# Kernel optimization log

Hardware: AMD Instinct MI355X
Metric: run time of the kernel (lower is better)

Reference implementation:

```python
import jax, jax.numpy as jnp
import numpy as np

TILE = 16
CLIP_NEAR, CLIP_FAR = 0.01, 10.0


def _sqrt_keepnan(x):
    # forward: sqrt(x) for x>0, NaN otherwise (matches torch.sqrt on negatives);
    # double-where keeps gradients finite.
    pos = x > 0
    return jnp.where(pos, jnp.sqrt(jnp.where(pos, x, 1.0)), jnp.nan)


def _quat_to_rot(q):
    # faithful to the source _quat_to_rot (including its sign quirks)
    x, y, z, w = q[:, 0], q[:, 1], q[:, 2], q[:, 3]
    r0 = jnp.stack([1 - 2 * (y * y + z * z), 2 * (x * y - w * z), 2 * (x * z + w * y)], -1)
    r1 = jnp.stack([2 * (x * y + w * z), 1 - 2 * (x * x - z * z), 2 * (y * z - w * x)], -1)
    r2 = jnp.stack([2 * (x * z + w * y), 2 * (y * z + w * x), 1 - 2 * (x * x + y * y)], -1)
    return jnp.stack([r0, r1, r2], -2)  # (N,3,3)


def _forward(mu, scales, quats, cols, opcs, viewmat, focal, H, W):
    N = mu.shape[0]
    fx = fy = float(focal)
    cx, cy = W / 2.0, H / 2.0
    n_, f_ = CLIP_NEAR, CLIP_FAR

    # --- project gaussians ---
    t = viewmat @ jnp.concatenate([mu.T, jnp.ones((1, N), mu.dtype)], 0)  # (4,N) camera space
    tp0 = (2.0 * fx / W) * t[0]
    tp1 = (2.0 * fy / H) * t[1]
    tp2 = ((f_ + n_) / (f_ - n_)) * t[2] + (-2.0 * f_ * n_ / (f_ - n_)) * t[3]
    tp3 = t[2]
    xys = jnp.stack([W * tp0 / tp3 / 2 + cx, H * tp1 / tp3 / 2 + cy], 1)  # (N,2)
    depths = tp2

    R = _quat_to_rot(quats)
    RS = R * scales[:, None, :]              # R @ diag(s)
    Sigma = RS @ jnp.swapaxes(RS, 1, 2)      # (N,3,3)
    tz = t[2]
    zz = jnp.zeros_like(tz)
    J = jnp.stack([
        jnp.stack([fx / tz, zz, -fx * t[0] / tz ** 2], -1),
        jnp.stack([zz, fy / tz, -fy * t[1] / tz ** 2], -1)], -2)  # (N,2,3)
    Rcw = viewmat[:3, :3]
    M = jnp.einsum('nij,jk->nik', J, Rcw)
    covs = jnp.einsum('nij,njk,nlk->nil', M, Sigma, M)  # (N,2,2)

    ind = jnp.argsort(depths)                # depth sort (front-to-back)
    xys, covs = xys[ind], covs[ind]
    cols_s, opcs_s = cols[ind], opcs[ind]

    # --- bounding boxes -> tile membership mask ---
    a, b, d = covs[:, 0, 0], covs[:, 0, 1], covs[:, 1, 1]
    Aev = jnp.sqrt(a * a - 2 * a * d + 4 * b * b + d * d)
    Bev = a + d
    l1, l2 = 0.5 * (Aev + Bev), 0.5 * (Bev - Aev)
    r1 = 3.0 * _sqrt_keepnan(l1)
    r2 = 3.0 * _sqrt_keepnan(l2)
    mx, my = xys[:, 0], xys[:, 1]
    corners = jnp.stack([
        jnp.stack([mx - r1, my + r2], -1),
        jnp.stack([mx + r1, my + r2], -1),
        jnp.stack([mx + r1, my - r2], -1),
        jnp.stack([mx - r1, my - r2], -1)], 1)  # (N,4,2)
    theta = jnp.where(b != 0, jnp.arctan2(l1 - a, b),
                      jnp.where(a >= d, jnp.pi / 2, 0.0))
    cth, sth = jnp.cos(theta), jnp.sin(theta)
    rot = jnp.stack([jnp.stack([cth, -sth], -1), jnp.stack([sth, cth], -1)], -2)
    bm = corners.mean(1, keepdims=True)
    bbs = jnp.einsum('nij,nkj->nki', rot, corners - bm) + bm
    bbs = jnp.where(jnp.isnan(bbs), -1.0, bbs)
    Wt, Ht = W // TILE, H // TILE
    xmin = jnp.clip(jnp.floor(bbs[:, :, 0].min(1) / TILE), 0, Wt - 1).astype(jnp.int32)
    xmax = jnp.clip(jnp.ceil(bbs[:, :, 0].max(1) / TILE), 0, Wt - 1).astype(jnp.int32)
    ymin = jnp.clip(jnp.floor(bbs[:, :, 1].min(1) / TILE), 0, Ht - 1).astype(jnp.int32)
    ymax = jnp.clip(jnp.ceil(bbs[:, :, 1].max(1) / TILE), 0, Ht - 1).astype(jnp.int32)
    txi = jnp.arange(Wt)
    tyi = jnp.arange(Ht)
    tmask = ((txi[None, None, :] >= xmin[:, None, None]) & (txi[None, None, :] <= xmax[:, None, None]) &
             (tyi[None, :, None] >= ymin[:, None, None]) & (tyi[None, :, None] <= ymax[:, None, None]))  # (N,Ht,Wt)
    pmask = jnp.moveaxis(jnp.repeat(jnp.repeat(tmask, TILE, 1), TILE, 2), 0, -1)  # (H,W,N)

    # --- rasterize: per-pixel gaussian eval + sorted alpha compositing ---
    e = 1e-6
    det = (a + e) * (d + e) - covs[:, 0, 1] * covs[:, 1, 0]
    i00 = (d + e) / det
    i01 = -covs[:, 0, 1] / det
    i10 = -covs[:, 1, 0] / det
    i11 = (a + e) / det
    px = jnp.arange(W, dtype=mu.dtype)
    py = jnp.arange(H, dtype=mu.dtype)
    dx = px[None, :, None] - mx[None, None, :]   # (1,W,N)
    dy = py[:, None, None] - my[None, None, :]   # (H,1,N)
    quad = dx * (i00 * dx + i01 * dy) + dy * (i10 * dx + i11 * dy)  # (H,W,N)
    Pg = jnp.nan_to_num(jnp.exp(-0.5 * quad))
    O = jax.nn.sigmoid(jax.nn.sigmoid(opcs_s))   # double sigmoid: faithful to source
    alpha = O[None, None, :] * Pg
    alpha = jnp.where(pmask, alpha, 0.0)         # only gaussians binned to this tile
    alpha = jnp.where(alpha < 0.001, 0.0, alpha)
    alpha = jnp.minimum(alpha, 0.99)
    trans = jnp.cumprod(1.0 - alpha, -1)         # inclusive transmittance
    Dtr = jnp.concatenate([jnp.ones((H, W, 1), alpha.dtype), trans[..., :-1]], -1)
    C = jnp.clip(cols_s, 1e-4, 1.0)
    rgb = jnp.clip(jnp.einsum('hwn,nc->hwc', alpha * Dtr, C), 1e-4, 1.0)
    nonempty = jnp.repeat(jnp.repeat(tmask.any(0), TILE, 0), TILE, 1)  # empty tiles stay 0
    return jnp.where(nonempty[..., None], rgb, 0.0)


def setup_inputs() -> dict:
    key = jax.random.key(0)
    ks = jax.random.split(key, 6)
    N, H, W = 512, 256, 256
    mu = jax.random.normal(ks[0], (N, 3), jnp.float32)
    scales = jax.random.uniform(ks[1], (N, 3), jnp.float32) * 0.05 + 0.01
    q = jax.random.normal(ks[2], (N, 4), jnp.float32)
    quats = q / jnp.linalg.norm(q, axis=1, keepdims=True)
    cols = jax.random.uniform(ks[3], (N, 3), jnp.float32)
    opcs = jax.random.normal(ks[4], (N,), jnp.float32)
    viewmat = jnp.array([[1, 0, 0, 0], [0, 1, 0, 0], [0, 0, 1, 5.0], [0, 0, 0, 1]], jnp.float32)
    gt = jax.random.uniform(ks[5], (H, W, 3), jnp.float32)
    return {"mu": mu, "scales": scales, "quats": quats, "cols": cols, "opcs": opcs,
            "viewmat": viewmat, "gt": gt, "focal": 200, "H": H, "W": W}


def reference(mu, scales, quats, cols, opcs, viewmat, gt, focal, H, W):
    # gt is accepted (matches source signature) but unused by forward
    return _forward(mu, scales, quats, cols, opcs, viewmat, focal, H, W)
```

## Files before the change

kernel.cpp:

```cpp
#include <hip/hip_runtime.h>
#include <math.h>
#include <float.h>

#define NMAX 512
#define TILE 16
#define FDIV(a,b) __fdividef((a),(b))

__global__ __launch_bounds__(1024) void fused_kernel(
    const float* __restrict__ mu, const float* __restrict__ scales,
    const float* __restrict__ quats, const float* __restrict__ cols,
    const float* __restrict__ opcs, const float* __restrict__ vm,
    const int* __restrict__ focal_p, const int* __restrict__ H_p,
    const int* __restrict__ W_p, float* __restrict__ out, int N)
{
    __shared__ float s_mx[NMAX], s_my[NMAX];
    __shared__ float s_q00[NMAX], s_qs[NMAX], s_q11[NMAX];
    __shared__ float s_O[NMAX], s_c0[NMAX], s_c1[NMAX], s_c2[NMAX];
    __shared__ float4 s_rs0[NMAX], s_rs1[NMAX], s_rs2[NMAX];
    __shared__ unsigned long long s_lk[NMAX];
    __shared__ int s_ord[NMAX];
    __shared__ float4 s_part[3][256];
    __shared__ int s_bc[16];

    const int lt = threadIdx.x;
    const int lane = lt & 63, w = lt >> 6;
    const int tx = blockIdx.x, ty = blockIdx.y;

    const int   Wi = W_p[0], Hi = H_p[0];
    const float fx = (float)focal_p[0];
    const float fy = fx;
    const float Wf = (float)Wi, Hf = (float)Hi;
    const float cxf = (float)((double)Wi / 2.0);
    const float cyf = (float)((double)Hi / 2.0);
    const float sxc = (float)(2.0 * (double)fx / (double)Wi);
    const float syc = (float)(2.0 * (double)fy / (double)Hi);
    const float dc1 = (float)((10.0 + 0.01) / (10.0 - 0.01));
    const float dc2 = (float)(-2.0 * 10.0 * 0.01 / (10.0 - 0.01));
    const int Wt = Wi / TILE, Ht = Hi / TILE;

    bool covered = false;
    unsigned int key = 0;
    float t0, t1, t2, M00, M01, M02, M10, M11, M12, mx, my;

    if (lt >= 512) {
        const int g2 = lt - 512;
        if (g2 < N) {
            const float4 q = ((const float4*)quats)[g2];
            const float qx = q.x, qy = q.y, qz = q.z, qw = q.w;
            const float R00 = 1.0f - 2.0f*(qy*qy + qz*qz);
            const float R01 = 2.0f*(qx*qy - qw*qz);
            const float R02 = 2.0f*(qx*qz + qw*qy);
            const float R10 = 2.0f*(qx*qy + qw*qz);
            const float R11 = 1.0f - 2.0f*(qx*qx - qz*qz);
            const float R12 = 2.0f*(qy*qz - qw*qx);
            const float R20 = 2.0f*(qx*qz + qw*qy);
            const float R21 = 2.0f*(qy*qz + qw*qx);
            const float R22 = 1.0f - 2.0f*(qx*qx + qy*qy);

            const float s0 = scales[3*g2], s1 = scales[3*g2+1], s2 = scales[3*g2+2];
            s_rs0[g2] = make_float4(R00*s0, R01*s1, R02*s2, 0.0f);
            s_rs1[g2] = make_float4(R10*s0, R11*s1, R12*s2, 0.0f);
            s_rs2[g2] = make_float4(R20*s0, R21*s1, R22*s2, 0.0f);

            const float op  = opcs[g2];
            const float sg1 = FDIV(1.0f, 1.0f + __expf(-op));
            s_O [g2] = FDIV(1.0f, 1.0f + __expf(-sg1));
            s_c0[g2] = fminf(fmaxf(cols[3*g2    ], 1e-04f), 1.0f);
            s_c1[g2] = fminf(fmaxf(cols[3*g2 + 1], 1e-04f), 1.0f);
            s_c2[g2] = fminf(fmaxf(cols[3*g2 + 2], 1e-04f), 1.0f);
        }
    } else {
        const int g = lt;
        if (g < N) {
            const float m0 = mu[3*g], m1 = mu[3*g+1], m2 = mu[3*g+2];
            t0 = vm[0]*m0  + vm[1]*m1  + vm[2]*m2  + vm[3];
            t1 = vm[4]*m0  + vm[5]*m1  + vm[6]*m2  + vm[7];
            t2 = vm[8]*m0  + vm[9]*m1  + vm[10]*m2 + vm[11];
            const float t3 = vm[12]*m0 + vm[13]*m1 + vm[14]*m2 + vm[15];

            const float depth = dc1 * t2 + dc2 * t3;
            unsigned int ub = __float_as_uint(depth);
            key = (ub & 0x80000000u) ? ~ub : (ub | 0x80000000u);

            const float itz = FDIV(1.0f, t2);
            mx = (Wf * (sxc * t0)) * itz * 0.5f + cxf;
            my = (Hf * (syc * t1)) * itz * 0.5f + cyf;

            const float J00 = fx * itz;
            const float J02 = -fx * t0 * itz * itz;
            const float J11 = fy * itz;
            const float J12 = -fy * t1 * itz * itz;
            M00 = J00*vm[0] + J02*vm[8];
            M01 = J00*vm[1] + J02*vm[9];
            M02 = J00*vm[2] + J02*vm[10];
            M10 = J11*vm[4] + J12*vm[8];
            M11 = J11*vm[5] + J12*vm[9];
            M12 = J11*vm[6] + J12*vm[10];
        }
    }
    __syncthreads();

    if (lt < 512 && lt < N) {
        const int g = lt;
        const float4 A0 = s_rs0[g], A1 = s_rs1[g], A2 = s_rs2[g];
        const float B00 = M00*A0.x + M01*A1.x + M02*A2.x;
        const float B01 = M00*A0.y + M01*A1.y + M02*A2.y;
        const float B02 = M00*A0.z + M01*A1.z + M02*A2.z;
        const float B10 = M10*A0.x + M11*A1.x + M12*A2.x;
        const float B11 = M10*A0.y + M11*A1.y + M12*A2.y;
        const float B12 = M10*A0.z + M11*A1.z + M12*A2.z;
        const float a = B00*B00 + B01*B01 + B02*B02;
        const float b = B00*B10 + B01*B11 + B02*B12;
        const float d = B10*B10 + B11*B11 + B12*B12;

        const float Aev = sqrtf(a*a - 2.0f*a*d + 4.0f*b*b + d*d);
        const float Bev = a + d;
        const float l1 = 0.5f * (Aev + Bev);
        const float l2 = 0.5f * (Bev - Aev);
        const float r1 = (l1 > 0.0f) ? 3.0f * sqrtf(l1) : NAN;
        const float r2 = (l2 > 0.0f) ? 3.0f * sqrtf(l2) : NAN;

        float cth, sth;
        if (b != 0.0f) {
            const float yv = l1 - a;
            const float ih = __frsqrt_rn(b*b + yv*yv);
            cth = b  * ih;
            sth = yv * ih;
        } else if (a >= d) {
            cth = -4.371139e-8f;
            sth = 1.0f;
        } else {
            cth = 1.0f;
            sth = 0.0f;
        }

        const float u  = mx - r1, v  = mx + r1;
        const float r_ = my + r2, s_ = my - r2;
        const float bmx = (((u + v) + v) + u) * 0.25f;
        const float bmy = (((r_ + r_) + s_) + s_) * 0.25f;
        const float pxo = u - bmx, qxo = v - bmx;
        const float ryo = r_ - bmy, syo = s_ - bmy;

        const float Axp = cth * pxo, Axq = cth * qxo;
        const float Bxr = (-sth) * ryo, Bxs = (-sth) * syo;
        float xmn  = (fminf(Axp, Axq) + fminf(Bxr, Bxs)) + bmx;
        float xmxv = (fmaxf(Axp, Axq) + fmaxf(Bxr, Bxs)) + bmx;
        const float Ayp = sth * pxo, Ayq = sth * qxo;
        const float Byr = cth * ryo, Bys = cth * syo;
        float ymn  = (fminf(Ayp, Ayq) + fminf(Byr, Bys)) + bmy;
        float ymxv = (fmaxf(Ayp, Ayq) + fmaxf(Byr, Bys)) + bmy;
        if (isnan(xmxv)) { xmn = -1.0f; xmxv = -1.0f; }
        if (isnan(ymxv)) { ymn = -1.0f; ymxv = -1.0f; }

        const int xmin = (int)fminf(fmaxf(floorf(xmn  * 0.0625f), 0.0f), (float)(Wt - 1));
        const int xmax = (int)fminf(fmaxf(ceilf (xmxv * 0.0625f), 0.0f), (float)(Wt - 1));
        const int ymin = (int)fminf(fmaxf(floorf(ymn  * 0.0625f), 0.0f), (float)(Ht - 1));
        const int ymax = (int)fminf(fmaxf(ceilf (ymxv * 0.0625f), 0.0f), (float)(Ht - 1));

        const float e = 1e-06f;
        const float det = (a + e) * (d + e) - b * b;
        const float idet = FDIV(1.0f, det);

        s_mx [g] = mx;
        s_my [g] = my;
        s_q00[g] = -0.5f * (d + e) * idet;
        s_qs [g] = b * idet;
        s_q11[g] = -0.5f * (a + e) * idet;

        covered = (tx >= xmin) & (tx <= xmax) & (ty >= ymin) & (ty <= ymax);
    }

    const unsigned long long word = __ballot(covered);
    if (lane == 0) s_bc[w] = __popcll(word);
    __syncthreads();

    int base = 0, M = 0;
    #pragma unroll
    for (int i = 0; i < 16; ++i) {
        const int c = s_bc[i];
        if (i < w) base += c;
        M += c;
    }
    if (covered) {
        const int rank = base + __popcll(word & ((1ull << lane) - 1ull));
        s_lk[rank] = ((unsigned long long)key << 32) | (unsigned int)lt;
    }
    __syncthreads();

    for (int t = lt; t < M; t += 1024) {
        const unsigned long long mine = s_lk[t];
        int rank = 0;
        for (int s = 0; s < M; ++s) rank += (s_lk[s] < mine) ? 1 : 0;
        s_ord[rank] = (int)(mine & 0xFFFFFFFFu);
    }
    __syncthreads();

    const int p  = lt & 255;
    const int qd = lt >> 8;
    const int W  = gridDim.x * TILE;
    const int px = tx * TILE + (p & 15);
    const int py = ty * TILE + (p >> 4);
    const float fpx = (float)px, fpy = (float)py;

    const int Mq = (M + 3) >> 2;
    const int j0 = qd * Mq;
    const int j1 = min(M, j0 + Mq);

    float Tt = 1.0f, rr = 0.0f, gg = 0.0f, bb = 0.0f;
    for (int j = j0; j < j1; ++j) {
        const int n = s_ord[j];
        const float dx = fpx - s_mx[n];
        const float dy = fpy - s_my[n];
        const float qv = s_q00[n]*dx*dx + s_qs[n]*(dx*dy) + s_q11[n]*dy*dy;
        float Pg = __expf(qv);
        if (Pg != Pg) Pg = 0.0f;
        float alpha = s_O[n] * Pg;
        alpha = (alpha < 0.001f) ? 0.0f : fminf(alpha, 0.99f);
        const float wgt = alpha * Tt;
        rr = fmaf(wgt, s_c0[n], rr);
        gg = fmaf(wgt, s_c1[n], gg);
        bb = fmaf(wgt, s_c2[n], bb);
        Tt = fmaf(-alpha, Tt, Tt);
    }

    if (qd >= 1) s_part[qd - 1][p] = make_float4(rr, gg, bb, Tt);
    __syncthreads();

    if (qd == 0) {
        const float4 q1 = s_part[0][p];
        const float4 q2 = s_part[1][p];
        const float4 q3 = s_part[2][p];
        float cr = fmaf(q2.w, q3.x, q2.x);
        float cg = fmaf(q2.w, q3.y, q2.y);
        float cb = fmaf(q2.w, q3.z, q2.z);
        cr = fmaf(q1.w, cr, q1.x);
        cg = fmaf(q1.w, cg, q1.y);
        cb = fmaf(q1.w, cb, q1.z);
        rr = fmaf(Tt, cr, rr);
        gg = fmaf(Tt, cg, gg);
        bb = fmaf(Tt, cb, bb);

        const int o = (py * W + px) * 3;
        if (M > 0) {
            out[o    ] = fminf(fmaxf(rr, 1e-04f), 1.0f);
            out[o + 1] = fminf(fmaxf(gg, 1e-04f), 1.0f);
            out[o + 2] = fminf(fmaxf(bb, 1e-04f), 1.0f);
        } else {
            out[o] = 0.0f; out[o + 1] = 0.0f; out[o + 2] = 0.0f;
        }
    }
}

extern "C" void kernel_launch(void* const* d_in, const int* in_sizes, int n_in,
                              void* d_out, int out_size, void* d_ws, size_t ws_size,
                              hipStream_t stream) {
    const float* mu     = (const float*)d_in[0];
    const float* scales = (const float*)d_in[1];
    const float* quats  = (const float*)d_in[2];
    const float* cols   = (const float*)d_in[3];
    const float* opcs   = (const float*)d_in[4];
    const float* vm     = (const float*)d_in[5];
    const int* focal_p  = (const int*)d_in[7];
    const int* H_p      = (const int*)d_in[8];
    const int* W_p      = (const int*)d_in[9];

    const int N = in_sizes[4];
    const int HW = out_size / 3;
    int W = (int)(sqrt((double)HW) + 0.5);
    int H = HW / W;

    dim3 grid(W / TILE, H / TILE), block(1024);
    fused_kernel<<<grid, block, 0, stream>>>(mu, scales, quats, cols, opcs, vm,
                                             focal_p, H_p, W_p, (float*)d_out, N);
}
```

Baseline: 14.63 us.

## Pack sorted gaussian params into float4 records, fold opacity into exp2, early-exit empty tiles

After ranking, each covered gaussian's parameters are gathered into packed float4 records stored in depth order, reusing the rotation-scale buffer. The blend loop then does two or three vector shared loads per gaussian instead of an index lookup plus nine scattered scalar loads. Opacity is folded into the exponent as log2(O) and the quadratic coefficients are pre-scaled by log2(e), so one exp2 replaces an exp and a multiply. Blocks with no covered gaussians now write zeros and return before the sort. Folding opacity into the exponent changes rounding slightly.

```diff
diff --git a/kernel.cpp b/kernel.cpp
--- a/kernel.cpp
+++ b/kernel.cpp
@@ -5,6 +5,7 @@
 #define NMAX 512
 #define TILE 16
 #define FDIV(a,b) __fdividef((a),(b))
+#define LOG2E 1.4426950408889634f
 
 __global__ __launch_bounds__(1024) void fused_kernel(
     const float* __restrict__ mu, const float* __restrict__ scales,
@@ -15,10 +16,9 @@
 {
     __shared__ float s_mx[NMAX], s_my[NMAX];
     __shared__ float s_q00[NMAX], s_qs[NMAX], s_q11[NMAX];
-    __shared__ float s_O[NMAX], s_c0[NMAX], s_c1[NMAX], s_c2[NMAX];
-    __shared__ float4 s_rs0[NMAX], s_rs1[NMAX], s_rs2[NMAX];
+    __shared__ float s_lO[NMAX], s_c0[NMAX], s_c1[NMAX], s_c2[NMAX];
+    __shared__ float4 s_rs[NMAX][3];
     __shared__ unsigned long long s_lk[NMAX];
-    __shared__ int s_ord[NMAX];
     __shared__ float4 s_part[3][256];
     __shared__ int s_bc[16];
 
@@ -58,13 +58,14 @@
             const float R22 = 1.0f - 2.0f*(qx*qx + qy*qy);
 
             const float s0 = scales[3*g2], s1 = scales[3*g2+1], s2 = scales[3*g2+2];
-            s_rs0[g2] = make_float4(R00*s0, R01*s1, R02*s2, 0.0f);
-            s_rs1[g2] = make_float4(R10*s0, R11*s1, R12*s2, 0.0f);
-            s_rs2[g2] = make_float4(R20*s0, R21*s1, R22*s2, 0.0f);
+            s_rs[g2][0] = make_float4(R00*s0, R01*s1, R02*s2, 0.0f);
+            s_rs[g2][1] = make_float4(R10*s0, R11*s1, R12*s2, 0.0f);
+            s_rs[g2][2] = make_float4(R20*s0, R21*s1, R22*s2, 0.0f);
 
             const float op  = opcs[g2];
             const float sg1 = FDIV(1.0f, 1.0f + __expf(-op));
-            s_O [g2] = FDIV(1.0f, 1.0f + __expf(-sg1));
+            const float Ov  = FDIV(1.0f, 1.0f + __expf(-sg1));
+            s_lO[g2] = __log2f(Ov);
             s_c0[g2] = fminf(fmaxf(cols[3*g2    ], 1e-04f), 1.0f);
             s_c1[g2] = fminf(fmaxf(cols[3*g2 + 1], 1e-04f), 1.0f);
             s_c2[g2] = fminf(fmaxf(cols[3*g2 + 2], 1e-04f), 1.0f);
@@ -102,7 +103,7 @@
 
     if (lt < 512 && lt < N) {
         const int g = lt;
-        const float4 A0 = s_rs0[g], A1 = s_rs1[g], A2 = s_rs2[g];
+        const float4 A0 = s_rs[g][0], A1 = s_rs[g][1], A2 = s_rs[g][2];
         const float B00 = M00*A0.x + M01*A1.x + M02*A2.x;
         const float B01 = M00*A0.y + M01*A1.y + M02*A2.y;
         const float B02 = M00*A0.z + M01*A1.z + M02*A2.z;
@@ -163,9 +164,9 @@
 
         s_mx [g] = mx;
         s_my [g] = my;
-        s_q00[g] = -0.5f * (d + e) * idet;
-        s_qs [g] = b * idet;
-        s_q11[g] = -0.5f * (a + e) * idet;
+        s_q00[g] = (-0.5f * LOG2E) * (d + e) * idet;
+        s_qs [g] = LOG2E * b * idet;
+        s_q11[g] = (-0.5f * LOG2E) * (a + e) * idet;
 
         covered = (tx >= xmin) & (tx <= xmax) & (ty >= ymin) & (ty <= ymax);
     }
@@ -181,45 +182,59 @@
         if (i < w) base += c;
         M += c;
     }
-    if (covered) {
-        const int rank = base + __popcll(word & ((1ull << lane) - 1ull));
-        s_lk[rank] = ((unsigned long long)key << 32) | (unsigned int)lt;
-    }
-    __syncthreads();
-
-    for (int t = lt; t < M; t += 1024) {
-        const unsigned long long mine = s_lk[t];
-        int rank = 0;
-        for (int s = 0; s < M; ++s) rank += (s_lk[s] < mine) ? 1 : 0;
-        s_ord[rank] = (int)(mine & 0xFFFFFFFFu);
-    }
-    __syncthreads();
 
     const int p  = lt & 255;
     const int qd = lt >> 8;
     const int W  = gridDim.x * TILE;
     const int px = tx * TILE + (p & 15);
     const int py = ty * TILE + (p >> 4);
+
+    if (M == 0) {
+        if (qd == 0) {
+            const int o = (py * W + px) * 3;
+            out[o] = 0.0f; out[o + 1] = 0.0f; out[o + 2] = 0.0f;
+        }
+        return;
+    }
+
+    if (covered) {
+        const int rank = base + __popcll(word & ((1ull << lane) - 1ull));
+        s_lk[rank] = ((unsigned long long)key << 32) | (unsigned int)lt;
+    }
+    __syncthreads();
+
+    for (int t = lt; t < M; t += 1024) {
+        const unsigned long long mine = s_lk[t];
+        int rank = 0;
+        for (int s = 0; s < M; ++s) rank += (s_lk[s] < mine) ? 1 : 0;
+        const int n = (int)(mine & 0xFFFFFFFFu);
+        s_rs[rank][0] = make_float4(s_mx[n], s_my[n], s_q00[n], s_qs[n]);
+        s_rs[rank][1] = make_float4(s_q11[n], s_lO[n], s_c0[n], s_c1[n]);
+        s_rs[rank][2] = make_float4(s_c2[n], 0.0f, 0.0f, 0.0f);
+    }
+    __syncthreads();
+
     const float fpx = (float)px, fpy = (float)py;
-
     const int Mq = (M + 3) >> 2;
     const int j0 = qd * Mq;
     const int j1 = min(M, j0 + Mq);
 
     float Tt = 1.0f, rr = 0.0f, gg = 0.0f, bb = 0.0f;
     for (int j = j0; j < j1; ++j) {
-        const int n = s_ord[j];
-        const float dx = fpx - s_mx[n];
-        const float dy = fpy - s_my[n];
-        const float qv = s_q00[n]*dx*dx + s_qs[n]*(dx*dy) + s_q11[n]*dy*dy;
-        float Pg = __expf(qv);
-        if (Pg != Pg) Pg = 0.0f;
-        float alpha = s_O[n] * Pg;
-        alpha = (alpha < 0.001f) ? 0.0f : fminf(alpha, 0.99f);
+        const float4 r0 = s_rs[j][0];
+        const float4 r1 = s_rs[j][1];
+        const float  c2 = s_rs[j][2].x;
+
+        const float dx = fpx - r0.x;
+        const float dy = fpy - r0.y;
+        const float ex = r0.z*(dx*dx) + r0.w*(dx*dy) + r1.x*(dy*dy) + r1.y;
+        float a2 = exp2f(ex);
+        if (a2 != a2) a2 = 0.0f;
+        const float alpha = (a2 < 0.001f) ? 0.0f : fminf(a2, 0.99f);
         const float wgt = alpha * Tt;
-        rr = fmaf(wgt, s_c0[n], rr);
-        gg = fmaf(wgt, s_c1[n], gg);
-        bb = fmaf(wgt, s_c2[n], bb);
+        rr = fmaf(wgt, r1.z, rr);
+        gg = fmaf(wgt, r1.w, gg);
+        bb = fmaf(wgt, c2, bb);
         Tt = fmaf(-alpha, Tt, Tt);
     }
 
@@ -241,13 +256,9 @@
         bb = fmaf(Tt, cb, bb);
 
         const int o = (py * W + px) * 3;
-        if (M > 0) {
-            out[o    ] = fminf(fmaxf(rr, 1e-04f), 1.0f);
-            out[o + 1] = fminf(fmaxf(gg, 1e-04f), 1.0f);
-            out[o + 2] = fminf(fmaxf(bb, 1e-04f), 1.0f);
-        } else {
-            out[o] = 0.0f; out[o + 1] = 0.0f; out[o + 2] = 0.0f;
-        }
+        out[o    ] = fminf(fmaxf(rr, 1e-04f), 1.0f);
+        out[o + 1] = fminf(fmaxf(gg, 1e-04f), 1.0f);
+        out[o + 2] = fminf(fmaxf(bb, 1e-04f), 1.0f);
     }
 }
 
```

Result: no change. 14.62 us (-0.0%).
